# Kernel tuning notes

Measured on AMD Instinct MI355X. Metric: run time of the kernel, lower is better.

## Reference

```python
import jax, jax.numpy as jnp
import numpy as np


def setup_inputs() -> dict:
    key = jax.random.key(0)
    ks = jax.random.split(key, 8)
    B, N, K, C_in, M, C_add, C_out = 2, 40000, 16, 64, 16, 3, 128
    in_features = (C_in + C_add) * M  # 1072
    input_features = jax.random.normal(ks[0], (B, N, C_in), dtype=jnp.float32)
    neighbor_inds = jax.random.randint(ks[1], (B, N, K), 0, N, dtype=jnp.int64)
    inverse_neighbors = jax.random.randint(ks[2], (B, N * K), 0, N * K, dtype=jnp.int64)
    inverse_k = jax.random.randint(ks[3], (B, N * K), 0, K, dtype=jnp.int64)
    inverse_idx = jax.random.randint(ks[4], (B, N * K), 0, N, dtype=jnp.int64)
    weightnet = jax.random.normal(ks[5], (B, N, K, M), dtype=jnp.float32)
    additional_features = jax.random.normal(ks[6], (B, N, K, C_add), dtype=jnp.float32)
    bound = 1.0 / np.sqrt(in_features)
    kw, kb = jax.random.split(ks[7])
    linear_weight = jax.random.uniform(kw, (C_out, in_features), dtype=jnp.float32, minval=-bound, maxval=bound)
    linear_bias = jax.random.uniform(kb, (C_out,), dtype=jnp.float32, minval=-bound, maxval=bound)
    return {
        "input_features": input_features,
        "neighbor_inds": neighbor_inds,
        "inverse_neighbors": inverse_neighbors,
        "inverse_k": inverse_k,
        "inverse_idx": inverse_idx,
        "weightnet": weightnet,
        "additional_features": additional_features,
        "linear_weight": linear_weight,
        "linear_bias": linear_bias,
    }


def reference(input_features, neighbor_inds, inverse_neighbors, inverse_k, inverse_idx,
              weightnet, additional_features, linear_weight, linear_bias):
    # inverse_* tensors are only used by the custom CUDA backward; unused here.
    B, N, K = neighbor_inds.shape
    # gather neighbor features: [B, N, K, C_in]
    gathered = jnp.take_along_axis(input_features[:, :, None, :],
                                   neighbor_inds[..., None], axis=1)
    # concat extra per-neighbor features -> [B, N, K, C]
    feats = jnp.concatenate([gathered, additional_features], axis=-1)
    # PConv: [B,N,C,K] @ [B,N,K,M] -> [B,N,C,M] -> flatten to [B,N,C*M]
    pconv = jnp.einsum('bnkc,bnkm->bncm', feats, weightnet)
    pconv = pconv.reshape(B, N, -1)
    # fused linear
    out = jnp.einsum('bnf,of->bno', pconv, linear_weight) + linear_bias
    return out
```

## Files before the change

### kernel.cpp

```cpp
#include <hip/hip_runtime.h>
#include <stdint.h>

typedef unsigned short u16;
typedef short short8 __attribute__((ext_vector_type(8)));
typedef float floatx4 __attribute__((ext_vector_type(4)));

#define NPERB   40000
#define NPTS    80000
#define KNBR    16
#define CIN     64
#define MDIM    16
#define CADD    3
#define CF      (CIN + CADD)
#define COUT    128
#define KF      1072
#define KP      1088
#define NKT     34
#define PTSB    16
#define SLAB    65
#define GR      128
#define PPB     8

__device__ __forceinline__ u16 f2bf(float f) {
    union { float f; unsigned int u; } v; v.f = f;
    unsigned int u = v.u;
    return (u16)((u + 0x7FFFu + ((u >> 16) & 1u)) >> 16);
}
__device__ __forceinline__ short8 pack8(floatx4 x, floatx4 y) {
    union { short8 v; u16 a[8]; } u;
    u.a[0] = f2bf(x[0]); u.a[1] = f2bf(x[1]); u.a[2] = f2bf(x[2]); u.a[3] = f2bf(x[3]);
    u.a[4] = f2bf(y[0]); u.a[5] = f2bf(y[1]); u.a[6] = f2bf(y[2]); u.a[7] = f2bf(y[3]);
    return u.v;
}
__device__ __forceinline__ unsigned swz(unsigned chunk) {
    return chunk ^ ((chunk >> 3) & 7u);
}
__device__ __forceinline__ void gload_lds16(const void* g, void* l) {
    __builtin_amdgcn_global_load_lds(
        (const __attribute__((address_space(1))) void*)g,
        (__attribute__((address_space(3))) void*)l, 16, 0, 0);
}

__global__ void prep_lw_kernel(const float* __restrict__ lw, u16* __restrict__ lwp) {
    int i = blockIdx.x * 256 + threadIdx.x;
    if (i >= COUT * KP) return;
    int o = i / KP, f = i - o * KP;
    lwp[i] = (f < KF) ? f2bf(lw[(size_t)o * KF + f]) : (u16)0;
}

__device__ __forceinline__ void emit_point(
    int lane, float av, const float (&fv)[KNBR], const float* wl,
    u16* __restrict__ dst)
{
    const int em = lane & 15, ec = lane >> 4;
    float ev = 0.f;
#pragma unroll
    for (int k = 0; k < KNBR; k++)
        ev += __shfl(av, k * CADD + ec) * wl[k * MDIM + em];
    if (ec == 3) ev = 0.f;
    dst[1024 + lane] = f2bf(ev);

    floatx4 a0 = 0, a1 = 0, a2 = 0, a3 = 0;
#pragma unroll
    for (int k = 0; k < KNBR; k++) {
        const floatx4* w4 = (const floatx4*)(wl + k * MDIM);
        const float fvk = fv[k];
        a0 += fvk * w4[0]; a1 += fvk * w4[1];
        a2 += fvk * w4[2]; a3 += fvk * w4[3];
    }
    *(short8*)(dst + lane * 16)     = pack8(a0, a1);
    *(short8*)(dst + lane * 16 + 8) = pack8(a2, a3);
}

__global__ __launch_bounds__(256) void pconv_kernel(
    const float* __restrict__ inp,
    const int*   __restrict__ nbr,
    const float* __restrict__ wn,
    const float* __restrict__ addl,
    u16* __restrict__ pc)
{
    __shared__ __align__(16) float Wns[PPB * KNBR * MDIM];

    const int wave = threadIdx.x >> 6;
    const int lane = threadIdx.x & 63;
    const int pbase = blockIdx.x * PPB;
    const float* inpb = inp + ((pbase >= NPERB) ? (size_t)NPERB * CIN : 0);

    const int pr0 = wave * 2;
    const int p0  = __builtin_amdgcn_readfirstlane(pbase + pr0);
    const int p1  = p0 + 1;

    float* wl0 = Wns + pr0 * (KNBR * MDIM);
    float* wl1 = wl0 + KNBR * MDIM;
    gload_lds16(wn + (size_t)p0 * (KNBR * MDIM) + lane * 4, wl0);
    gload_lds16(wn + (size_t)p1 * (KNBR * MDIM) + lane * 4, wl1);

    float av0 = (lane < KNBR * CADD) ? addl[(size_t)p0 * (KNBR * CADD) + lane] : 0.f;
    float av1 = (lane < KNBR * CADD) ? addl[(size_t)p1 * (KNBR * CADD) + lane] : 0.f;

    const int* nb0 = nbr + (size_t)p0 * KNBR;
    const int* nb1 = nbr + (size_t)p1 * KNBR;
    int idx0[KNBR], idx1[KNBR];
#pragma unroll
    for (int k = 0; k < KNBR; k++) idx0[k] = nb0[k];
#pragma unroll
    for (int k = 0; k < KNBR; k++) idx1[k] = nb1[k];

    float fv0[KNBR], fv1[KNBR];
#pragma unroll
    for (int k = 0; k < KNBR; k++) fv0[k] = inpb[(size_t)idx0[k] * CIN + lane];
#pragma unroll
    for (int k = 0; k < KNBR; k++) fv1[k] = inpb[(size_t)idx1[k] * CIN + lane];

    asm volatile("s_waitcnt vmcnt(0)" ::: "memory");
    __builtin_amdgcn_sched_barrier(0);

    emit_point(lane, av0, fv0, wl0, pc + (size_t)p0 * KP);
    emit_point(lane, av1, fv1, wl1, pc + (size_t)p1 * KP);
}

__global__ __launch_bounds__(256) void gemm_kernel(
    const u16* __restrict__ pc,
    const u16* __restrict__ lwp,
    const float* __restrict__ bias,
    float* __restrict__ out)
{
    const int wave = threadIdx.x >> 6;
    const int lane = threadIdx.x & 63;
    const int r16 = lane & 15, quad = lane >> 4;
    const int row0 = blockIdx.x * GR + wave * 32;

    const u16* pA0 = pc + (size_t)(row0 + r16) * KP + quad * 8;
    const u16* pA1 = pA0 + (size_t)16 * KP;
    const u16* pB  = lwp + (size_t)r16 * KP + quad * 8;

    floatx4 acc0[8], acc1[8];
#pragma unroll
    for (int n = 0; n < 8; n++) { acc0[n] = 0; acc1[n] = 0; }

    short8 Ac0, Ac1, Bc[8];
    short8 An0, An1, Bn[8];
    Ac0 = *(const short8*)pA0;
    Ac1 = *(const short8*)pA1;
#pragma unroll
    for (int n = 0; n < 8; n++)
        Bc[n] = *(const short8*)(pB + (size_t)n * 16 * KP);

    for (int kt = 0; kt + 1 < NKT; kt += 2) {
        An0 = *(const short8*)(pA0 + (kt + 1) * 32);
        An1 = *(const short8*)(pA1 + (kt + 1) * 32);
#pragma unroll
        for (int n = 0; n < 8; n++)
            Bn[n] = *(const short8*)(pB + (size_t)n * 16 * KP + (kt + 1) * 32);
#pragma unroll
        for (int n = 0; n < 8; n++) {
            acc0[n] = __builtin_amdgcn_mfma_f32_16x16x32_bf16(Ac0, Bc[n], acc0[n], 0, 0, 0);
            acc1[n] = __builtin_amdgcn_mfma_f32_16x16x32_bf16(Ac1, Bc[n], acc1[n], 0, 0, 0);
        }
        if (kt + 2 < NKT) {
            Ac0 = *(const short8*)(pA0 + (kt + 2) * 32);
            Ac1 = *(const short8*)(pA1 + (kt + 2) * 32);
#pragma unroll
            for (int n = 0; n < 8; n++)
                Bc[n] = *(const short8*)(pB + (size_t)n * 16 * KP + (kt + 2) * 32);
        }
#pragma unroll
        for (int n = 0; n < 8; n++) {
            acc0[n] = __builtin_amdgcn_mfma_f32_16x16x32_bf16(An0, Bn[n], acc0[n], 0, 0, 0);
            acc1[n] = __builtin_amdgcn_mfma_f32_16x16x32_bf16(An1, Bn[n], acc1[n], 0, 0, 0);
        }
    }

#pragma unroll
    for (int n = 0; n < 8; n++) {
        const float bv = bias[n * 16 + r16];
#pragma unroll
        for (int r = 0; r < 4; r++) {
            size_t row = (size_t)(row0 + quad * 4 + r) * COUT;
            out[row + n * 16 + r16] = acc0[n][r] + bv;
            row = (size_t)(row0 + 16 + quad * 4 + r) * COUT;
            out[row + n * 16 + r16] = acc1[n][r] + bv;
        }
    }
}

__device__ __forceinline__ void compute_point(
    int pr, int lane, float av, const float (&fv)[KNBR],
    const float* wl, u16* Apc)
{
    const int em = lane & 15, ec = lane >> 4;
    float ev = 0.f;
#pragma unroll
    for (int k = 0; k < KNBR; k++)
        ev += __shfl(av, k * CADD + ec) * wl[k * MDIM + em];
    if (ec == 3) ev = 0.f;
    {
        unsigned kt   = 32 + (lane >> 5);
        unsigned quad = (lane >> 3) & 3;
        unsigned ch   = kt * SLAB + (unsigned)pr * 4 + quad;
        Apc[swz(ch) * 8 + (lane & 7)] = f2bf(ev);
    }
    floatx4 a0 = 0, a1 = 0, a2 = 0, a3 = 0;
#pragma unroll
    for (int k = 0; k < KNBR; k++) {
        const floatx4* w4 = (const floatx4*)(wl + k * MDIM);
        const float fvk = fv[k];
        a0 += fvk * w4[0]; a1 += fvk * w4[1];
        a2 += fvk * w4[2]; a3 += fvk * w4[3];
    }
    {
        unsigned kt = lane >> 1, qb = (lane & 1) * 2;
        unsigned ch = kt * SLAB + (unsigned)pr * 4 + qb;
        *(short8*)&Apc[swz(ch) * 8]     = pack8(a0, a1);
        *(short8*)&Apc[swz(ch + 1) * 8] = pack8(a2, a3);
    }
}

__global__ __launch_bounds__(512, 6) void fused_kernel(
    const float* __restrict__ inp, const int* __restrict__ nbr,
    const float* __restrict__ wn, const float* __restrict__ addl,
    const u16* __restrict__ lwp, const float* __restrict__ bias,
    float* __restrict__ out)
{
    __shared__ __align__(16) u16   Apc[(NKT * SLAB + 8) * 8];
    __shared__ __align__(16) float Wns[PTSB * KNBR * MDIM];

    const int wave = threadIdx.x >> 6;
    const int lane = threadIdx.x & 63;
    const int pbase = blockIdx.x * PTSB;
    const float* inpb = inp + ((pbase >= NPERB) ? (size_t)NPERB * CIN : 0);

    const int pr0 = wave * 2;
    const int p0  = __builtin_amdgcn_readfirstlane(pbase + pr0);
    const int p1  = p0 + 1;

    float* wl0 = Wns + pr0 * (KNBR * MDIM);
    float* wl1 = wl0 + KNBR * MDIM;
    gload_lds16(wn + (size_t)p0 * (KNBR * MDIM) + lane * 4, wl0);
    gload_lds16(wn + (size_t)p1 * (KNBR * MDIM) + lane * 4, wl1);

    float av0 = (lane < KNBR * CADD) ? addl[(size_t)p0 * (KNBR * CADD) + lane] : 0.f;
    float av1 = (lane < KNBR * CADD) ? addl[(size_t)p1 * (KNBR * CADD) + lane] : 0.f;

    const int* nb0 = nbr + (size_t)p0 * KNBR;
    const int* nb1 = nbr + (size_t)p1 * KNBR;
    int idx0[KNBR], idx1[KNBR];
#pragma unroll
    for (int k = 0; k < KNBR; k++) idx0[k] = nb0[k];
#pragma unroll
    for (int k = 0; k < KNBR; k++) idx1[k] = nb1[k];

    float fv0[KNBR], fv1[KNBR];
#pragma unroll
    for (int k = 0; k < KNBR; k++) fv0[k] = inpb[(size_t)idx0[k] * CIN + lane];
#pragma unroll
    for (int k = 0; k < KNBR; k++) fv1[k] = inpb[(size_t)idx1[k] * CIN + lane];

    asm volatile("s_waitcnt vmcnt(0)" ::: "memory");
    __builtin_amdgcn_sched_barrier(0);

    compute_point(pr0,     lane, av0, fv0, wl0, Apc);
    compute_point(pr0 + 1, lane, av1, fv1, wl1, Apc);

    const int r16 = lane & 15, quad = lane >> 4;
    const int c0 = wave * 16;
    const u16* Bp = lwp + (size_t)(c0 + r16) * KP + quad * 8;
    const unsigned abase = (unsigned)r16 * 4 + quad;
    const float bv = bias[c0 + r16];

    __syncthreads();

    floatx4 acc = 0;
#pragma unroll 2
    for (int kt = 0; kt < NKT; kt++) {
        short8 A = *(const short8*)&Apc[swz((unsigned)kt * SLAB + abase) * 8];
        short8 B = *(const short8*)(Bp + kt * 32);
        acc = __builtin_amdgcn_mfma_f32_16x16x32_bf16(A, B, acc, 0, 0, 0);
    }

#pragma unroll
    for (int r = 0; r < 4; r++) {
        const size_t row = (size_t)(pbase + quad * 4 + r) * COUT;
        out[row + c0 + r16] = acc[r] + bv;
    }
}

__global__ __launch_bounds__(256) void fused_fallback_kernel(
    const float* __restrict__ inp, const int* __restrict__ nbr,
    const float* __restrict__ wn, const float* __restrict__ addl,
    const float* __restrict__ lw, const float* __restrict__ bias,
    float* __restrict__ out)
{
    const int p = blockIdx.x;
    const int b = p / NPERB;
    const int tid = threadIdx.x;
    __shared__ float sf[KNBR * CF];
    __shared__ float sw[KNBR * MDIM];
    __shared__ float sp[KF];

    sw[tid] = wn[(size_t)p * (KNBR * MDIM) + tid];
    for (int i = tid; i < KNBR * CIN; i += 256) {
        int k = i >> 6, c = i & 63;
        int idx = nbr[(size_t)p * KNBR + k];
        sf[k * CF + c] = inp[((size_t)b * NPERB + idx) * CIN + c];
    }
    if (tid < KNBR * CADD) {
        int k = tid / CADD, c = tid - k * CADD;
        sf[k * CF + CIN + c] = addl[(size_t)p * (KNBR * CADD) + tid];
    }
    __syncthreads();
    for (int f = tid; f < KF; f += 256) {
        int c = f >> 4, m = f & 15;
        float s = 0;
#pragma unroll
        for (int k = 0; k < KNBR; k++) s += sf[k * CF + c] * sw[k * MDIM + m];
        sp[f] = s;
    }
    __syncthreads();
    const int o = tid >> 1, h = tid & 1;
    float s = 0;
    for (int f = h * (KF / 2); f < (h + 1) * (KF / 2); f++)
        s += sp[f] * lw[(size_t)o * KF + f];
    s += __shfl_xor(s, 1);
    if (h == 0) out[(size_t)p * COUT + o] = s + bias[o];
}

extern "C" void kernel_launch(void* const* d_in, const int* in_sizes, int n_in,
                              void* d_out, int out_size, void* d_ws, size_t ws_size,
                              hipStream_t stream) {
    const float* inp  = (const float*)d_in[0];
    const int*   nbr  = (const int*)d_in[1];
    const float* wn   = (const float*)d_in[5];
    const float* addl = (const float*)d_in[6];
    const float* lw   = (const float*)d_in[7];
    const float* bias = (const float*)d_in[8];
    float* out = (float*)d_out;

    const size_t lw_bytes = (size_t)COUT * KP * sizeof(u16);
    const size_t pc_bytes = (size_t)NPTS * KP * sizeof(u16);

    if (ws_size >= lw_bytes + pc_bytes) {
        u16* lwp = (u16*)d_ws;
        u16* pcw = lwp + (size_t)COUT * KP;
        prep_lw_kernel<<<(COUT * KP + 255) / 256, 256, 0, stream>>>(lw, lwp);
        pconv_kernel<<<NPTS / PPB, 256, 0, stream>>>(inp, nbr, wn, addl, pcw);
        gemm_kernel<<<NPTS / GR, 256, 0, stream>>>(pcw, lwp, bias, out);
    } else if (ws_size >= lw_bytes) {
        u16* lwp = (u16*)d_ws;
        prep_lw_kernel<<<(COUT * KP + 255) / 256, 256, 0, stream>>>(lw, lwp);
        fused_kernel<<<NPTS / PTSB, 512, 0, stream>>>(inp, nbr, wn, addl, lwp, bias, out);
    } else {
        fused_fallback_kernel<<<NPTS, 256, 0, stream>>>(inp, nbr, wn, addl, lw, bias, out);
    }
}
```

Before: 343.7 us.

## Pipeline GEMM A-tile loads through LDS with multi-stage prefetch

The GEMM kernel now streams A fragments from global memory into per-wave LDS buffers using direct global-to-LDS loads, four stages deep. B fragments are held in a three-deep register ring, and the K loop is fully unrolled with explicit vmcnt waits so that memory latency overlaps MFMA work. Launch bounds now request two blocks per CU, and the bias loads move to the start of the kernel. The hand-tuned waitcnt counts are fragile if load counts change, and the larger register footprint may limit occupancy.

Measured after the change: 340.9 us. No clear change (-0.8%).

```diff
diff --git a/kernel.cpp b/kernel.cpp
--- a/kernel.cpp
+++ b/kernel.cpp
@@ -119,67 +119,88 @@
     emit_point(lane, av1, fv1, wl1, pc + (size_t)p1 * KP);
 }
 
-__global__ __launch_bounds__(256) void gemm_kernel(
+__global__ __launch_bounds__(256, 2) void gemm_kernel(
     const u16* __restrict__ pc,
     const u16* __restrict__ lwp,
     const float* __restrict__ bias,
     float* __restrict__ out)
 {
+    __shared__ __align__(16) u16 As[4][4][1024];
+
     const int wave = threadIdx.x >> 6;
     const int lane = threadIdx.x & 63;
     const int r16 = lane & 15, quad = lane >> 4;
     const int row0 = blockIdx.x * GR + wave * 32;
 
-    const u16* pA0 = pc + (size_t)(row0 + r16) * KP + quad * 8;
-    const u16* pA1 = pA0 + (size_t)16 * KP;
-    const u16* pB  = lwp + (size_t)r16 * KP + quad * 8;
+    const u16* aS0 = pc + (size_t)(row0 + r16) * KP + quad * 8;
+    const u16* aS1 = aS0 + (size_t)16 * KP;
+    u16* aD = &As[wave][0][0];
+
+    const u16* bB = lwp + (size_t)r16 * KP + quad * 8;
+
+    float bv[8];
+#pragma unroll
+    for (int n = 0; n < 8; n++) bv[n] = bias[n * 16 + r16];
+    __builtin_amdgcn_sched_barrier(0);
 
     floatx4 acc0[8], acc1[8];
 #pragma unroll
     for (int n = 0; n < 8; n++) { acc0[n] = 0; acc1[n] = 0; }
 
-    short8 Ac0, Ac1, Bc[8];
-    short8 An0, An1, Bn[8];
-    Ac0 = *(const short8*)pA0;
-    Ac1 = *(const short8*)pA1;
-#pragma unroll
-    for (int n = 0; n < 8; n++)
-        Bc[n] = *(const short8*)(pB + (size_t)n * 16 * KP);
-
-    for (int kt = 0; kt + 1 < NKT; kt += 2) {
-        An0 = *(const short8*)(pA0 + (kt + 1) * 32);
-        An1 = *(const short8*)(pA1 + (kt + 1) * 32);
-#pragma unroll
-        for (int n = 0; n < 8; n++)
-            Bn[n] = *(const short8*)(pB + (size_t)n * 16 * KP + (kt + 1) * 32);
-#pragma unroll
-        for (int n = 0; n < 8; n++) {
-            acc0[n] = __builtin_amdgcn_mfma_f32_16x16x32_bf16(Ac0, Bc[n], acc0[n], 0, 0, 0);
-            acc1[n] = __builtin_amdgcn_mfma_f32_16x16x32_bf16(Ac1, Bc[n], acc1[n], 0, 0, 0);
-        }
-        if (kt + 2 < NKT) {
-            Ac0 = *(const short8*)(pA0 + (kt + 2) * 32);
-            Ac1 = *(const short8*)(pA1 + (kt + 2) * 32);
-#pragma unroll
-            for (int n = 0; n < 8; n++)
-                Bc[n] = *(const short8*)(pB + (size_t)n * 16 * KP + (kt + 2) * 32);
-        }
-#pragma unroll
-        for (int n = 0; n < 8; n++) {
-            acc0[n] = __builtin_amdgcn_mfma_f32_16x16x32_bf16(An0, Bn[n], acc0[n], 0, 0, 0);
-            acc1[n] = __builtin_amdgcn_mfma_f32_16x16x32_bf16(An1, Bn[n], acc1[n], 0, 0, 0);
-        }
-    }
+    short8 Bq[3][8];
+
+#define STAGE(s) { \
+    gload_lds16(aS0 + (s) * 32, aD + ((s) & 3) * 1024); \
+    gload_lds16(aS1 + (s) * 32, aD + ((s) & 3) * 1024 + 512); }
+
+#define LOADB(s) { \
+    _Pragma("unroll") \
+    for (int n = 0; n < 8; n++) \
+        Bq[(s) % 3][n] = *(const short8*)(bB + (size_t)n * 16 * KP + (s) * 32); }
+
+    STAGE(0); STAGE(1); STAGE(2);
+    __builtin_amdgcn_sched_barrier(0);
+    LOADB(0);
+    __builtin_amdgcn_sched_barrier(0);
+    LOADB(1);
+    __builtin_amdgcn_sched_barrier(0);
+
+#define STEP(kt, N) { \
+    if ((kt) + 3 < NKT) STAGE((kt) + 3); \
+    if ((kt) + 2 < NKT) LOADB((kt) + 2); \
+    __builtin_amdgcn_sched_barrier(0); \
+    asm volatile("s_waitcnt vmcnt(" #N ")"); \
+    __builtin_amdgcn_sched_barrier(0); \
+    short8 A0 = *(const short8*)(aD + ((kt) & 3) * 1024 + lane * 8); \
+    short8 A1 = *(const short8*)(aD + ((kt) & 3) * 1024 + 512 + lane * 8); \
+    asm volatile("s_waitcnt lgkmcnt(0)"); \
+    __builtin_amdgcn_sched_barrier(0); \
+    _Pragma("unroll") \
+    for (int n = 0; n < 8; n++) { \
+        acc0[n] = __builtin_amdgcn_mfma_f32_16x16x32_bf16(A0, Bq[(kt) % 3][n], acc0[n], 0, 0, 0); \
+        acc1[n] = __builtin_amdgcn_mfma_f32_16x16x32_bf16(A1, Bq[(kt) % 3][n], acc1[n], 0, 0, 0); \
+    } }
+
+    STEP(0, 18)  STEP(1, 20)  STEP(2, 20)  STEP(3, 20)  STEP(4, 20)
+    STEP(5, 20)  STEP(6, 20)  STEP(7, 20)  STEP(8, 20)  STEP(9, 20)
+    STEP(10, 20) STEP(11, 20) STEP(12, 20) STEP(13, 20) STEP(14, 20)
+    STEP(15, 20) STEP(16, 20) STEP(17, 20) STEP(18, 20) STEP(19, 20)
+    STEP(20, 20) STEP(21, 20) STEP(22, 20) STEP(23, 20) STEP(24, 20)
+    STEP(25, 20) STEP(26, 20) STEP(27, 20) STEP(28, 20) STEP(29, 20)
+    STEP(30, 20) STEP(31, 18) STEP(32, 8)  STEP(33, 0)
+
+#undef STEP
+#undef LOADB
+#undef STAGE
 
 #pragma unroll
     for (int n = 0; n < 8; n++) {
-        const float bv = bias[n * 16 + r16];
 #pragma unroll
         for (int r = 0; r < 4; r++) {
             size_t row = (size_t)(row0 + quad * 4 + r) * COUT;
-            out[row + n * 16 + r16] = acc0[n][r] + bv;
+            out[row + n * 16 + r16] = acc0[n][r] + bv[n];
             row = (size_t)(row0 + 16 + quad * 4 + r) * COUT;
-            out[row + n * 16 + r16] = acc1[n][r] + bv;
+            out[row + n * 16 + r16] = acc1[n][r] + bv[n];
         }
     }
 }
```
